# Performance work log

Measured on AMD Instinct MI355X. Metric: run time of the kernel, lower is better.

The kernel has to match this reference:

```python
import jax, jax.numpy as jnp
import numpy as np

N = 100000   # nodes
M = N - 1    # tree edges (child -> parent)
EMB = 512    # embedding_size
ENC = 512    # encoder_size


def setup_inputs() -> dict:
    key = jax.random.key(0)
    ks = jax.random.split(key, 10)
    x = jax.random.normal(ks[0], (N, EMB), jnp.float32)
    h = jax.random.normal(ks[1], (N, ENC), jnp.float32)
    c = jax.random.normal(ks[2], (N, ENC), jnp.float32)
    child_idx = jax.random.randint(ks[3], (M,), 0, N)
    parent_idx = jax.random.randint(ks[4], (M,), 0, N)
    s = 0.05
    W_iou = jax.random.normal(ks[5], (3 * ENC, EMB), jnp.float32) * s
    U_iou = jax.random.normal(ks[6], (3 * ENC, ENC), jnp.float32) * s
    b_iou = jnp.zeros((3 * ENC,), jnp.float32)
    U_f_w = jax.random.normal(ks[7], (ENC, ENC), jnp.float32) * s
    U_f_b = jax.random.normal(ks[8], (ENC,), jnp.float32) * s
    return {"x": x, "h": h, "c": c, "child_idx": child_idx,
            "parent_idx": parent_idx, "W_iou": W_iou, "U_iou": U_iou,
            "b_iou": b_iou, "U_f_w": U_f_w, "U_f_b": U_f_b}


def reference(x, h, c, child_idx, parent_idx, W_iou, U_iou, b_iou, U_f_w, U_f_b):
    n = x.shape[0]
    # message_func: gather child states along edges  [M, ENC]
    h_src = h[child_idx]
    c_src = c[child_idx]
    # reduce_func: forget gate per child, ragged sums over children
    f = jax.nn.sigmoid(h_src @ U_f_w.T + U_f_b)               # [M, ENC]
    h_tilde = jax.ops.segment_sum(h_src, parent_idx, num_segments=n)
    c_red = jax.ops.segment_sum(f * c_src, parent_idx, num_segments=n)
    deg = jax.ops.segment_sum(jnp.ones((h_src.shape[0],), x.dtype),
                              parent_idx, num_segments=n)
    has_child = (deg > 0)[:, None]
    # reduce_func overwrites iou with U_iou(h_tilde) for nodes with children;
    # leaves keep the initial W_iou(x).
    iou = jnp.where(has_child, h_tilde @ U_iou.T, x @ W_iou.T) + b_iou
    i, o, u = jnp.split(iou, 3, axis=1)
    c_new = jax.nn.sigmoid(i) * jnp.tanh(u) + jnp.where(has_child, c_red, 0.0)
    h_new = jax.nn.sigmoid(o) * jnp.tanh(c_new)
    return h_new, c_new
```

## Files before the change

kernel.cpp:

```cpp
#include <hip/hip_runtime.h>
#include <stdint.h>

typedef __bf16 bf16x8 __attribute__((ext_vector_type(8)));
typedef float f32x4 __attribute__((ext_vector_type(4)));
typedef unsigned short ushort8 __attribute__((ext_vector_type(8)));

__device__ __forceinline__ float bf2f(unsigned short u) {
  union { uint32_t i; float f; } v; v.i = ((uint32_t)u) << 16; return v.f;
}
__device__ __forceinline__ unsigned short f2bf(float f) {
  union { uint32_t i; float f; } v; v.f = f;
  uint32_t u = v.i;
  return (unsigned short)((u + 0x7fffu + ((u >> 16) & 1u)) >> 16);
}
__device__ __forceinline__ float sigm(float x) { return 1.0f / (1.0f + __expf(-x)); }
__device__ __forceinline__ float tanh_f(float x) { return 1.0f - 2.0f / (__expf(2.0f * x) + 1.0f); }

__device__ __forceinline__ ushort4 cvt4(float4 a) {
  ushort4 o; o.x = f2bf(a.x); o.y = f2bf(a.y); o.z = f2bf(a.z); o.w = f2bf(a.w); return o;
}

__device__ __forceinline__ int xcd_swz(int bid, int nwg) {
  int q = nwg >> 3, r = nwg & 7;
  int x = bid & 7, idx = bid >> 3;
  return (x < r ? x * (q + 1) : r * (q + 1) + (x - r) * q) + idx;
}

__global__ void k_f2bf(const float* __restrict__ src, unsigned short* __restrict__ dst, long long n8) {
  long long t = (long long)blockIdx.x * blockDim.x + threadIdx.x;
  if (t >= n8) return;
  const float4* s = (const float4*)src + t * 2;
  float4 a = s[0], b = s[1];
  ((ushort4*)dst)[t * 2]     = cvt4(a);
  ((ushort4*)dst)[t * 2 + 1] = cvt4(b);
}

__global__ void k_hist(const int* __restrict__ parent, int* __restrict__ deg, int M) {
  int e = blockIdx.x * blockDim.x + threadIdx.x;
  if (e < M) atomicAdd(&deg[parent[e]], 1);
}

__global__ void k_scan1(const int* __restrict__ deg, unsigned long long* __restrict__ ps,
                        unsigned long long* __restrict__ bsum, int Nn) {
  __shared__ unsigned long long tmp[256];
  int t = blockIdx.x * 256 + threadIdx.x;
  int d = (t < Nn) ? deg[t] : 0;
  unsigned long long v = (unsigned long long)(unsigned)d | ((d > 0) ? (1ull << 32) : 0ull);
  tmp[threadIdx.x] = v;
  __syncthreads();
#pragma unroll
  for (int s = 1; s < 256; s <<= 1) {
    unsigned long long a = (threadIdx.x >= (unsigned)s) ? tmp[threadIdx.x - s] : 0;
    __syncthreads();
    tmp[threadIdx.x] += a;
    __syncthreads();
  }
  if (t < Nn) ps[t] = tmp[threadIdx.x] - v;
  if (threadIdx.x == 255) bsum[blockIdx.x] = tmp[255];
}

__global__ void k_scan2(unsigned long long* __restrict__ bsum, int nb,
                        int* __restrict__ meta, int Nn) {
  __shared__ unsigned long long tmp[512];
  int i = threadIdx.x;
  unsigned long long v = (i < nb) ? bsum[i] : 0;
  tmp[i] = v;
  __syncthreads();
#pragma unroll
  for (int s = 1; s < 512; s <<= 1) {
    unsigned long long a = (i >= s) ? tmp[i - s] : 0;
    __syncthreads();
    tmp[i] += a;
    __syncthreads();
  }
  if (i < nb) bsum[i] = tmp[i] - v;
  if (i == 511) {
    int Ni = (int)(tmp[511] >> 32);
    int L0 = ((Ni + 127) >> 7) << 7;
    meta[0] = Ni;
    meta[1] = L0;
    meta[2] = L0 + (Nn - Ni);
  }
}

__global__ void k_scan3(const unsigned long long* __restrict__ ps,
                        const unsigned long long* __restrict__ bsum,
                        const int* __restrict__ meta, const int* __restrict__ deg,
                        int* __restrict__ rs, int* __restrict__ cursor,
                        int* __restrict__ slot, int Nn) {
  int t = blockIdx.x * 256 + threadIdx.x;
  if (t >= Nn) return;
  unsigned long long p = ps[t] + bsum[blockIdx.x];
  int r  = (int)(p & 0xffffffffull);
  int si = (int)(p >> 32);
  rs[t] = r;
  cursor[t] = r;
  slot[t] = (deg[t] > 0) ? si : (meta[1] + (t - si));
}

__global__ void k_fill(const int* __restrict__ parent, const int* __restrict__ child,
                       int* __restrict__ cursor, int* __restrict__ childlist, int M) {
  int e = blockIdx.x * blockDim.x + threadIdx.x;
  if (e >= M) return;
  int p = parent[e];
  int pos = atomicAdd(&cursor[p], 1);
  childlist[pos] = child[e];
}

__global__ void k_reduce(const unsigned short* __restrict__ hbuf, const float* __restrict__ c,
                         const unsigned short* __restrict__ g, const float* __restrict__ x,
                         const int* __restrict__ rs, const int* __restrict__ childlist,
                         const int* __restrict__ slot,
                         unsigned short* __restrict__ Zp, unsigned short* __restrict__ credb,
                         int Nn, int M) {
  int p = blockIdx.x * 4 + (threadIdx.x >> 6);
  if (p >= Nn) return;
  int ln = threadIdx.x & 63;
  int j = ln * 8;
  int start = rs[p];
  int end = (p + 1 < Nn) ? rs[p + 1] : M;
  size_t zb = (size_t)slot[p] * 512 + j;
  if (end > start) {
    float hs[8] = {0, 0, 0, 0, 0, 0, 0, 0};
    float cs[8] = {0, 0, 0, 0, 0, 0, 0, 0};
    for (int i = start; i < end; ++i) {
      int ch = childlist[i];
      size_t cb = (size_t)ch * 512 + j;
      ushort8 hv = *(const ushort8*)(hbuf + cb);
      ushort8 gv = *(const ushort8*)(g + cb);
      float4 cv0 = *(const float4*)(c + cb);
      float4 cv1 = *(const float4*)(c + cb + 4);
      float cvf[8] = {cv0.x, cv0.y, cv0.z, cv0.w, cv1.x, cv1.y, cv1.z, cv1.w};
#pragma unroll
      for (int q = 0; q < 8; ++q) {
        hs[q] += bf2f(hv[q]);
        cs[q] += bf2f(gv[q]) * cvf[q];
      }
    }
    float4 h0 = {hs[0], hs[1], hs[2], hs[3]}, h1 = {hs[4], hs[5], hs[6], hs[7]};
    float4 c0 = {cs[0], cs[1], cs[2], cs[3]}, c1 = {cs[4], cs[5], cs[6], cs[7]};
    ((ushort4*)(Zp + zb))[0] = cvt4(h0);
    ((ushort4*)(Zp + zb))[1] = cvt4(h1);
    size_t cr = (size_t)p * 512 + j;
    ((ushort4*)(credb + cr))[0] = cvt4(c0);
    ((ushort4*)(credb + cr))[1] = cvt4(c1);
  } else {
    const float4* s = (const float4*)(x + (size_t)p * 512 + j);
    float4 x0 = s[0], x1 = s[1];
    ((ushort4*)(Zp + zb))[0] = cvt4(x0);
    ((ushort4*)(Zp + zb))[1] = cvt4(x1);
  }
}

template <int ACT>
__global__ __launch_bounds__(256)
void k_gemm_bt(const unsigned short* __restrict__ A, int K,
               const unsigned short* __restrict__ Bt,
               const float* __restrict__ bias,
               unsigned short* __restrict__ C, int ldc, int Mrows, int nbx) {
  __shared__ __align__(16) unsigned short ldsA[128 * 32];
  __shared__ __align__(16) unsigned short ldsB[128 * 32];
  const int tid = threadIdx.x;
  const int wv = tid >> 6, ln = tid & 63;
  const int wr = wv >> 1, wc = wv & 1;
  int wg = xcd_swz(blockIdx.x, gridDim.x);
  int rowp = wg / nbx;
  int colp = wg - rowp * nbx;
  const int row0 = rowp * 128;
  const int col0 = colp * 128;

  f32x4 acc[4][4] = {};

  for (int k0 = 0; k0 < K; k0 += 32) {
#pragma unroll
    for (int rep = 0; rep < 2; ++rep) {
      int cidx = rep * 256 + wv * 64 + ln;
      int r  = cidx >> 2;
      int kp = (cidx & 3) * 8;
      int ga = row0 + r; if (ga > Mrows - 1) ga = Mrows - 1;
      const unsigned short* srcA = A + (size_t)ga * K + k0 + kp;
      __builtin_amdgcn_global_load_lds(
          (const __attribute__((address_space(1))) void*)(void*)srcA,
          (__attribute__((address_space(3))) void*)(ldsA + (rep * 256 + wv * 64) * 8),
          16, 0, 0);
      const unsigned short* srcB = Bt + (size_t)(col0 + r) * K + k0 + kp;
      __builtin_amdgcn_global_load_lds(
          (const __attribute__((address_space(1))) void*)(void*)srcB,
          (__attribute__((address_space(3))) void*)(ldsB + (rep * 256 + wv * 64) * 8),
          16, 0, 0);
    }
    __syncthreads();

    bf16x8 af[4], bfr[4];
#pragma unroll
    for (int mi = 0; mi < 4; ++mi)
      af[mi] = *(const bf16x8*)(ldsA + (wr * 64 + mi * 16 + (ln & 15)) * 32 + (ln >> 4) * 8);
#pragma unroll
    for (int ni = 0; ni < 4; ++ni)
      bfr[ni] = *(const bf16x8*)(ldsB + (wc * 64 + ni * 16 + (ln & 15)) * 32 + (ln >> 4) * 8);
#pragma unroll
    for (int mi = 0; mi < 4; ++mi)
#pragma unroll
      for (int ni = 0; ni < 4; ++ni)
        acc[mi][ni] = __builtin_amdgcn_mfma_f32_16x16x32_bf16(af[mi], bfr[ni], acc[mi][ni], 0, 0, 0);
    __syncthreads();
  }

#pragma unroll
  for (int mi = 0; mi < 4; ++mi) {
#pragma unroll
    for (int ni = 0; ni < 4; ++ni) {
      int col = col0 + wc * 64 + ni * 16 + (ln & 15);
      float bv = bias[col];
#pragma unroll
      for (int r = 0; r < 4; ++r) {
        int m = row0 + wr * 64 + mi * 16 + (ln >> 4) * 4 + r;
        if (m < Mrows) {
          float v = acc[mi][ni][r] + bv;
          if (ACT == 1) v = sigm(v);
          C[(size_t)m * ldc + col] = f2bf(v);
        }
      }
    }
  }
}

__global__ __launch_bounds__(256)
void k_gemm_iou(const unsigned short* __restrict__ Zp,
                const unsigned short* __restrict__ Ub,
                const unsigned short* __restrict__ Wb,
                const float* __restrict__ bias,
                const int* __restrict__ meta,
                unsigned short* __restrict__ C) {
  __shared__ __align__(16) unsigned short ldsA[128 * 32];
  __shared__ __align__(16) unsigned short ldsB[128 * 32];
  const int K = 512, ldc = 1536;
  const int tid = threadIdx.x;
  const int wv = tid >> 6, ln = tid & 63;
  const int wr = wv >> 1, wc = wv & 1;
  int wg = xcd_swz(blockIdx.x, gridDim.x);
  int rowp = wg / 12;
  int colp = wg - rowp * 12;
  const int row0 = rowp * 128;
  const int col0 = colp * 128;

  const int Ni = meta[0], L0 = meta[1], lim2 = meta[2];
  const bool internal = row0 < L0;
  const int limit = internal ? Ni : lim2;
  if (row0 >= limit) return;
  const unsigned short* __restrict__ Bt = internal ? Ub : Wb;

  f32x4 acc[4][4] = {};

  for (int k0 = 0; k0 < K; k0 += 32) {
#pragma unroll
    for (int rep = 0; rep < 2; ++rep) {
      int cidx = rep * 256 + wv * 64 + ln;
      int r  = cidx >> 2;
      int kp = (cidx & 3) * 8;
      int ga = row0 + r; if (ga > limit - 1) ga = limit - 1;
      const unsigned short* srcA = Zp + (size_t)ga * K + k0 + kp;
      __builtin_amdgcn_global_load_lds(
          (const __attribute__((address_space(1))) void*)(void*)srcA,
          (__attribute__((address_space(3))) void*)(ldsA + (rep * 256 + wv * 64) * 8),
          16, 0, 0);
      const unsigned short* srcB = Bt + (size_t)(col0 + r) * K + k0 + kp;
      __builtin_amdgcn_global_load_lds(
          (const __attribute__((address_space(1))) void*)(void*)srcB,
          (__attribute__((address_space(3))) void*)(ldsB + (rep * 256 + wv * 64) * 8),
          16, 0, 0);
    }
    __syncthreads();

    bf16x8 af[4], bfr[4];
#pragma unroll
    for (int mi = 0; mi < 4; ++mi)
      af[mi] = *(const bf16x8*)(ldsA + (wr * 64 + mi * 16 + (ln & 15)) * 32 + (ln >> 4) * 8);
#pragma unroll
    for (int ni = 0; ni < 4; ++ni)
      bfr[ni] = *(const bf16x8*)(ldsB + (wc * 64 + ni * 16 + (ln & 15)) * 32 + (ln >> 4) * 8);
#pragma unroll
    for (int mi = 0; mi < 4; ++mi)
#pragma unroll
      for (int ni = 0; ni < 4; ++ni)
        acc[mi][ni] = __builtin_amdgcn_mfma_f32_16x16x32_bf16(af[mi], bfr[ni], acc[mi][ni], 0, 0, 0);
    __syncthreads();
  }

#pragma unroll
  for (int mi = 0; mi < 4; ++mi) {
#pragma unroll
    for (int ni = 0; ni < 4; ++ni) {
      int col = col0 + wc * 64 + ni * 16 + (ln & 15);
      float bv = bias[col];
#pragma unroll
      for (int r = 0; r < 4; ++r) {
        int m = row0 + wr * 64 + mi * 16 + (ln >> 4) * 4 + r;
        if (m < limit) {
          C[(size_t)m * ldc + col] = f2bf(acc[mi][ni][r] + bv);
        }
      }
    }
  }
}

__global__ void k_epilogue(const unsigned short* __restrict__ iou,
                           const unsigned short* __restrict__ credb,
                           const int* __restrict__ slot,
                           const int* __restrict__ meta,
                           float* __restrict__ out, int Nn) {
  long long t = (long long)blockIdx.x * blockDim.x + threadIdx.x;
  int n = (int)(t >> 6);
  if (n >= Nn) return;
  int j = ((int)t & 63) * 8;
  int sl = slot[n];
  int Ni = meta[0];
  size_t ib = (size_t)sl * 1536;
  ushort4 iv0 = *(const ushort4*)(iou + ib + j);
  ushort4 iv1 = *(const ushort4*)(iou + ib + j + 4);
  ushort4 ov0 = *(const ushort4*)(iou + ib + 512 + j);
  ushort4 ov1 = *(const ushort4*)(iou + ib + 512 + j + 4);
  ushort4 uv0 = *(const ushort4*)(iou + ib + 1024 + j);
  ushort4 uv1 = *(const ushort4*)(iou + ib + 1024 + j + 4);

  float carr[8] = {0, 0, 0, 0, 0, 0, 0, 0};
  if (sl < Ni) {
    size_t cr = (size_t)n * 512 + j;
    ushort4 c0 = *(const ushort4*)(credb + cr);
    ushort4 c1 = *(const ushort4*)(credb + cr + 4);
    carr[0] = bf2f(c0.x); carr[1] = bf2f(c0.y); carr[2] = bf2f(c0.z); carr[3] = bf2f(c0.w);
    carr[4] = bf2f(c1.x); carr[5] = bf2f(c1.y); carr[6] = bf2f(c1.z); carr[7] = bf2f(c1.w);
  }

  float iarr[8] = {bf2f(iv0.x), bf2f(iv0.y), bf2f(iv0.z), bf2f(iv0.w),
                   bf2f(iv1.x), bf2f(iv1.y), bf2f(iv1.z), bf2f(iv1.w)};
  float oarr[8] = {bf2f(ov0.x), bf2f(ov0.y), bf2f(ov0.z), bf2f(ov0.w),
                   bf2f(ov1.x), bf2f(ov1.y), bf2f(ov1.z), bf2f(ov1.w)};
  float uarr[8] = {bf2f(uv0.x), bf2f(uv0.y), bf2f(uv0.z), bf2f(uv0.w),
                   bf2f(uv1.x), bf2f(uv1.y), bf2f(uv1.z), bf2f(uv1.w)};
  float hn[8], cn[8];
#pragma unroll
  for (int q = 0; q < 8; ++q) {
    float cc = sigm(iarr[q]) * tanh_f(uarr[q]) + carr[q];
    cn[q] = cc;
    hn[q] = sigm(oarr[q]) * tanh_f(cc);
  }
  size_t hb = (size_t)n * 512 + j;
  size_t cb = (size_t)Nn * 512 + hb;
  *(float4*)(out + hb)     = make_float4(hn[0], hn[1], hn[2], hn[3]);
  *(float4*)(out + hb + 4) = make_float4(hn[4], hn[5], hn[6], hn[7]);
  *(float4*)(out + cb)     = make_float4(cn[0], cn[1], cn[2], cn[3]);
  *(float4*)(out + cb + 4) = make_float4(cn[4], cn[5], cn[6], cn[7]);
}

extern "C" void kernel_launch(void* const* d_in, const int* in_sizes, int n_in,
                              void* d_out, int out_size, void* d_ws, size_t ws_size,
                              hipStream_t stream) {
  const float* x     = (const float*)d_in[0];
  const float* h     = (const float*)d_in[1];
  const float* c     = (const float*)d_in[2];
  const int* child   = (const int*)d_in[3];
  const int* parent  = (const int*)d_in[4];
  const float* W_iou = (const float*)d_in[5];
  const float* U_iou = (const float*)d_in[6];
  const float* b_iou = (const float*)d_in[7];
  const float* U_f_w = (const float*)d_in[8];
  const float* U_f_b = (const float*)d_in[9];

  const int Nn = in_sizes[0] / 512;
  const int M  = in_sizes[3];

  float* out = (float*)d_out;

  char* ws = (char*)d_ws;
  auto al = [](size_t v) { return (v + 255) & ~(size_t)255; };
  size_t sz0    = al((size_t)(Nn + 256) * 1536 * 2);
  size_t offZp  = sz0;
  size_t szZp   = al((size_t)(Nn + 256) * 512 * 2);
  size_t offHb  = offZp + szZp;
  size_t szHb   = al((size_t)Nn * 512 * 2);
  size_t offCr  = offHb + szHb;
  size_t szCr   = al((size_t)Nn * 512 * 2);
  size_t offDeg = offCr + szCr;
  size_t szN4   = al((size_t)Nn * 4);
  size_t offRs  = offDeg + szN4;
  size_t offCur = offRs + szN4;
  size_t offSl  = offCur + szN4;
  size_t offPs  = offSl + szN4;
  size_t szPs   = al((size_t)Nn * 8);
  size_t offCl  = offPs + szPs;
  size_t szCl   = al((size_t)M * 4);
  size_t offBs  = offCl + szCl;
  size_t szBs   = al(512 * 8);
  size_t offMt  = offBs + szBs;
  size_t szMt   = 256;
  size_t offWf  = offMt + szMt;
  size_t szWf   = al(512 * 512 * 2);
  size_t offUb  = offWf + szWf;
  size_t szUw   = al((size_t)1536 * 512 * 2);
  size_t offWb  = offUb + szUw;
  size_t needed = offWb + szUw;
  if (ws_size < needed) return;

  unsigned short* g     = (unsigned short*)(ws);
  unsigned short* iou   = (unsigned short*)(ws);
  unsigned short* Zp    = (unsigned short*)(ws + offZp);
  unsigned short* hbuf  = (unsigned short*)(ws + offHb);
  unsigned short* credb = (unsigned short*)(ws + offCr);
  int*            deg   = (int*)(ws + offDeg);
  int*            rs    = (int*)(ws + offRs);
  int*            cursor= (int*)(ws + offCur);
  int*            slot  = (int*)(ws + offSl);
  unsigned long long* ps   = (unsigned long long*)(ws + offPs);
  int*            clist = (int*)(ws + offCl);
  unsigned long long* bsum = (unsigned long long*)(ws + offBs);
  int*            meta  = (int*)(ws + offMt);
  unsigned short* Wf    = (unsigned short*)(ws + offWf);
  unsigned short* Ub    = (unsigned short*)(ws + offUb);
  unsigned short* Wb    = (unsigned short*)(ws + offWb);

  hipMemsetAsync(deg, 0, (size_t)Nn * 4, stream);

  long long n8h = (long long)Nn * 512 / 8;
  k_f2bf<<<(int)((n8h + 255) / 256), 256, 0, stream>>>(h, hbuf, n8h);
  k_f2bf<<<(512 * 512 / 8 + 255) / 256, 256, 0, stream>>>(U_f_w, Wf, 512 * 512 / 8);
  k_f2bf<<<(1536 * 512 / 8 + 255) / 256, 256, 0, stream>>>(U_iou, Ub, 1536 * 512 / 8);
  k_f2bf<<<(1536 * 512 / 8 + 255) / 256, 256, 0, stream>>>(W_iou, Wb, 1536 * 512 / 8);

  int nb1 = (Nn + 255) / 256;
  k_hist<<<(M + 255) / 256, 256, 0, stream>>>(parent, deg, M);
  k_scan1<<<nb1, 256, 0, stream>>>(deg, ps, bsum, Nn);
  k_scan2<<<1, 512, 0, stream>>>(bsum, nb1, meta, Nn);
  k_scan3<<<nb1, 256, 0, stream>>>(ps, bsum, meta, deg, rs, cursor, slot, Nn);
  k_fill<<<(M + 255) / 256, 256, 0, stream>>>(parent, child, cursor, clist, M);

  int nbyF = (Nn + 127) / 128;
  k_gemm_bt<1><<<nbyF * 4, 256, 0, stream>>>(hbuf, 512, Wf, U_f_b, g, 512, Nn, 4);

  k_reduce<<<(Nn + 3) / 4, 256, 0, stream>>>(hbuf, c, g, x, rs, clist, slot, Zp, credb, Nn, M);

  int nbyI = (Nn >> 7) + 2;
  k_gemm_iou<<<nbyI * 12, 256, 0, stream>>>(Zp, Ub, Wb, b_iou, meta, iou);

  k_epilogue<<<(int)(((long long)Nn * 64 + 255) / 256), 256, 0, stream>>>(iou, credb, slot, meta, out, Nn);
}
```

Measured before the change: 775.6 us.

## Fuse gate epilogue into iou GEMM and pre-multiply forget gate by c

```diff
diff --git a/kernel.cpp b/kernel.cpp
--- a/kernel.cpp
+++ b/kernel.cpp
@@ -33,6 +33,19 @@
   float4 a = s[0], b = s[1];
   ((ushort4*)dst)[t * 2]     = cvt4(a);
   ((ushort4*)dst)[t * 2 + 1] = cvt4(b);
+}
+
+__global__ void k_build_bp(const float* __restrict__ src, unsigned short* __restrict__ bp, int total8) {
+  int t = blockIdx.x * blockDim.x + threadIdx.x;
+  if (t >= total8) return;
+  int R = t >> 6;
+  int ch = t & 63;
+  int g = R / 192, w = R - g * 192;
+  int srow = (w >> 6) * 512 + g * 64 + (w & 63);
+  const float4* s = (const float4*)(src + (size_t)srow * 512 + ch * 8);
+  unsigned short* d = bp + (size_t)R * 512 + ch * 8;
+  ((ushort4*)d)[0] = cvt4(s[0]);
+  ((ushort4*)d)[1] = cvt4(s[1]);
 }
 
 __global__ void k_hist(const int* __restrict__ parent, int* __restrict__ deg, int M) {
@@ -87,7 +100,7 @@
                         const unsigned long long* __restrict__ bsum,
                         const int* __restrict__ meta, const int* __restrict__ deg,
                         int* __restrict__ rs, int* __restrict__ cursor,
-                        int* __restrict__ slot, int Nn) {
+                        int* __restrict__ slot, int* __restrict__ nodeof, int Nn) {
   int t = blockIdx.x * 256 + threadIdx.x;
   if (t >= Nn) return;
   unsigned long long p = ps[t] + bsum[blockIdx.x];
@@ -95,7 +108,9 @@
   int si = (int)(p >> 32);
   rs[t] = r;
   cursor[t] = r;
-  slot[t] = (deg[t] > 0) ? si : (meta[1] + (t - si));
+  int sl = (deg[t] > 0) ? si : (meta[1] + (t - si));
+  slot[t] = sl;
+  nodeof[sl] = t;
 }
 
 __global__ void k_fill(const int* __restrict__ parent, const int* __restrict__ child,
@@ -107,8 +122,8 @@
   childlist[pos] = child[e];
 }
 
-__global__ void k_reduce(const unsigned short* __restrict__ hbuf, const float* __restrict__ c,
-                         const unsigned short* __restrict__ g, const float* __restrict__ x,
+__global__ void k_reduce(const unsigned short* __restrict__ hbuf,
+                         const unsigned short* __restrict__ fcb, const float* __restrict__ x,
                          const int* __restrict__ rs, const int* __restrict__ childlist,
                          const int* __restrict__ slot,
                          unsigned short* __restrict__ Zp, unsigned short* __restrict__ credb,
@@ -127,23 +142,19 @@
       int ch = childlist[i];
       size_t cb = (size_t)ch * 512 + j;
       ushort8 hv = *(const ushort8*)(hbuf + cb);
-      ushort8 gv = *(const ushort8*)(g + cb);
-      float4 cv0 = *(const float4*)(c + cb);
-      float4 cv1 = *(const float4*)(c + cb + 4);
-      float cvf[8] = {cv0.x, cv0.y, cv0.z, cv0.w, cv1.x, cv1.y, cv1.z, cv1.w};
+      ushort8 fv = *(const ushort8*)(fcb + cb);
 #pragma unroll
       for (int q = 0; q < 8; ++q) {
         hs[q] += bf2f(hv[q]);
-        cs[q] += bf2f(gv[q]) * cvf[q];
+        cs[q] += bf2f(fv[q]);
       }
     }
     float4 h0 = {hs[0], hs[1], hs[2], hs[3]}, h1 = {hs[4], hs[5], hs[6], hs[7]};
     float4 c0 = {cs[0], cs[1], cs[2], cs[3]}, c1 = {cs[4], cs[5], cs[6], cs[7]};
     ((ushort4*)(Zp + zb))[0] = cvt4(h0);
     ((ushort4*)(Zp + zb))[1] = cvt4(h1);
-    size_t cr = (size_t)p * 512 + j;
-    ((ushort4*)(credb + cr))[0] = cvt4(c0);
-    ((ushort4*)(credb + cr))[1] = cvt4(c1);
+    ((ushort4*)(credb + zb))[0] = cvt4(c0);
+    ((ushort4*)(credb + zb))[1] = cvt4(c1);
   } else {
     const float4* s = (const float4*)(x + (size_t)p * 512 + j);
     float4 x0 = s[0], x1 = s[1];
@@ -152,20 +163,20 @@
   }
 }
 
-template <int ACT>
 __global__ __launch_bounds__(256)
-void k_gemm_bt(const unsigned short* __restrict__ A, int K,
-               const unsigned short* __restrict__ Bt,
-               const float* __restrict__ bias,
-               unsigned short* __restrict__ C, int ldc, int Mrows, int nbx) {
+void k_gemm_f(const unsigned short* __restrict__ A,
+              const unsigned short* __restrict__ Bt,
+              const float* __restrict__ bias, const float* __restrict__ cmat,
+              unsigned short* __restrict__ C, int Mrows) {
   __shared__ __align__(16) unsigned short ldsA[128 * 32];
   __shared__ __align__(16) unsigned short ldsB[128 * 32];
+  const int K = 512, ldc = 512;
   const int tid = threadIdx.x;
   const int wv = tid >> 6, ln = tid & 63;
   const int wr = wv >> 1, wc = wv & 1;
   int wg = xcd_swz(blockIdx.x, gridDim.x);
-  int rowp = wg / nbx;
-  int colp = wg - rowp * nbx;
+  int rowp = wg >> 2;
+  int colp = wg & 3;
   const int row0 = rowp * 128;
   const int col0 = colp * 128;
 
@@ -216,8 +227,7 @@
       for (int r = 0; r < 4; ++r) {
         int m = row0 + wr * 64 + mi * 16 + (ln >> 4) * 4 + r;
         if (m < Mrows) {
-          float v = acc[mi][ni][r] + bv;
-          if (ACT == 1) v = sigm(v);
+          float v = sigm(acc[mi][ni][r] + bv) * cmat[(size_t)m * ldc + col];
           C[(size_t)m * ldc + col] = f2bf(v);
         }
       }
@@ -226,131 +236,105 @@
 }
 
 __global__ __launch_bounds__(256)
-void k_gemm_iou(const unsigned short* __restrict__ Zp,
-                const unsigned short* __restrict__ Ub,
-                const unsigned short* __restrict__ Wb,
-                const float* __restrict__ bias,
-                const int* __restrict__ meta,
-                unsigned short* __restrict__ C) {
+void k_gemm_iou_fused(const unsigned short* __restrict__ Zp,
+                      const unsigned short* __restrict__ BpU,
+                      const unsigned short* __restrict__ BpW,
+                      const float* __restrict__ bias,
+                      const int* __restrict__ meta,
+                      const int* __restrict__ nodeof,
+                      const unsigned short* __restrict__ credb,
+                      float* __restrict__ out, int Nn) {
   __shared__ __align__(16) unsigned short ldsA[128 * 32];
-  __shared__ __align__(16) unsigned short ldsB[128 * 32];
-  const int K = 512, ldc = 1536;
+  __shared__ __align__(16) unsigned short ldsB[192 * 32];
+  const int K = 512;
   const int tid = threadIdx.x;
   const int wv = tid >> 6, ln = tid & 63;
-  const int wr = wv >> 1, wc = wv & 1;
   int wg = xcd_swz(blockIdx.x, gridDim.x);
-  int rowp = wg / 12;
-  int colp = wg - rowp * 12;
+  int rowp = wg >> 3;
+  int colp = wg & 7;
   const int row0 = rowp * 128;
-  const int col0 = colp * 128;
+  const int enc0 = colp * 64;
 
   const int Ni = meta[0], L0 = meta[1], lim2 = meta[2];
   const bool internal = row0 < L0;
   const int limit = internal ? Ni : lim2;
   if (row0 >= limit) return;
-  const unsigned short* __restrict__ Bt = internal ? Ub : Wb;
-
-  f32x4 acc[4][4] = {};
+  const unsigned short* __restrict__ Bp = internal ? BpU : BpW;
+
+  f32x4 acc[2][12] = {};
 
   for (int k0 = 0; k0 < K; k0 += 32) {
 #pragma unroll
     for (int rep = 0; rep < 2; ++rep) {
-      int cidx = rep * 256 + wv * 64 + ln;
+      int cidx = rep * 256 + tid;
       int r  = cidx >> 2;
       int kp = (cidx & 3) * 8;
       int ga = row0 + r; if (ga > limit - 1) ga = limit - 1;
       const unsigned short* srcA = Zp + (size_t)ga * K + k0 + kp;
       __builtin_amdgcn_global_load_lds(
           (const __attribute__((address_space(1))) void*)(void*)srcA,
-          (__attribute__((address_space(3))) void*)(ldsA + (rep * 256 + wv * 64) * 8),
+          (__attribute__((address_space(3))) void*)(ldsA + (size_t)cidx * 8),
           16, 0, 0);
-      const unsigned short* srcB = Bt + (size_t)(col0 + r) * K + k0 + kp;
+    }
+#pragma unroll
+    for (int rep = 0; rep < 3; ++rep) {
+      int cidx = rep * 256 + tid;
+      int r  = cidx >> 2;
+      int kp = (cidx & 3) * 8;
+      const unsigned short* srcB = Bp + (size_t)(colp * 192 + r) * K + k0 + kp;
       __builtin_amdgcn_global_load_lds(
           (const __attribute__((address_space(1))) void*)(void*)srcB,
-          (__attribute__((address_space(3))) void*)(ldsB + (rep * 256 + wv * 64) * 8),
+          (__attribute__((address_space(3))) void*)(ldsB + (size_t)cidx * 8),
           16, 0, 0);
     }
     __syncthreads();
 
-    bf16x8 af[4], bfr[4];
-#pragma unroll
-    for (int mi = 0; mi < 4; ++mi)
-      af[mi] = *(const bf16x8*)(ldsA + (wr * 64 + mi * 16 + (ln & 15)) * 32 + (ln >> 4) * 8);
-#pragma unroll
-    for (int ni = 0; ni < 4; ++ni)
-      bfr[ni] = *(const bf16x8*)(ldsB + (wc * 64 + ni * 16 + (ln & 15)) * 32 + (ln >> 4) * 8);
-#pragma unroll
-    for (int mi = 0; mi < 4; ++mi)
-#pragma unroll
-      for (int ni = 0; ni < 4; ++ni)
+    bf16x8 af[2], bfr[12];
+#pragma unroll
+    for (int mi = 0; mi < 2; ++mi)
+      af[mi] = *(const bf16x8*)(ldsA + (wv * 32 + mi * 16 + (ln & 15)) * 32 + (ln >> 4) * 8);
+#pragma unroll
+    for (int ni = 0; ni < 12; ++ni)
+      bfr[ni] = *(const bf16x8*)(ldsB + (ni * 16 + (ln & 15)) * 32 + (ln >> 4) * 8);
+#pragma unroll
+    for (int mi = 0; mi < 2; ++mi)
+#pragma unroll
+      for (int ni = 0; ni < 12; ++ni)
         acc[mi][ni] = __builtin_amdgcn_mfma_f32_16x16x32_bf16(af[mi], bfr[ni], acc[mi][ni], 0, 0, 0);
     __syncthreads();
   }
 
-#pragma unroll
-  for (int mi = 0; mi < 4; ++mi) {
-#pragma unroll
-    for (int ni = 0; ni < 4; ++ni) {
-      int col = col0 + wc * 64 + ni * 16 + (ln & 15);
-      float bv = bias[col];
-#pragma unroll
-      for (int r = 0; r < 4; ++r) {
-        int m = row0 + wr * 64 + mi * 16 + (ln >> 4) * 4 + r;
-        if (m < limit) {
-          C[(size_t)m * ldc + col] = f2bf(acc[mi][ni][r] + bv);
-        }
+  float bi[4], bo[4], bu[4];
+#pragma unroll
+  for (int f = 0; f < 4; ++f) {
+    int enc = enc0 + f * 16 + (ln & 15);
+    bi[f] = bias[enc];
+    bo[f] = bias[512 + enc];
+    bu[f] = bias[1024 + enc];
+  }
+  const size_t cOff = (size_t)Nn * 512;
+#pragma unroll
+  for (int mi = 0; mi < 2; ++mi) {
+#pragma unroll
+    for (int r = 0; r < 4; ++r) {
+      int m = row0 + wv * 32 + mi * 16 + (ln >> 4) * 4 + r;
+      if (m >= limit) continue;
+      int node = nodeof[m];
+      size_t ob = (size_t)node * 512 + enc0 + (ln & 15);
+#pragma unroll
+      for (int f = 0; f < 4; ++f) {
+        float iv = acc[mi][f][r] + bi[f];
+        float ov = acc[mi][4 + f][r] + bo[f];
+        float uv = acc[mi][8 + f][r] + bu[f];
+        float cred = 0.0f;
+        if (internal) cred = bf2f(credb[(size_t)m * 512 + enc0 + f * 16 + (ln & 15)]);
+        float cc = sigm(iv) * tanh_f(uv) + cred;
+        float hn = sigm(ov) * tanh_f(cc);
+        out[ob + f * 16] = hn;
+        out[cOff + ob + f * 16] = cc;
       }
     }
   }
-}
-
-__global__ void k_epilogue(const unsigned short* __restrict__ iou,
-                           const unsigned short* __restrict__ credb,
-                           const int* __restrict__ slot,
-                           const int* __restrict__ meta,
-                           float* __restrict__ out, int Nn) {
-  long long t = (long long)blockIdx.x * blockDim.x + threadIdx.x;
-  int n = (int)(t >> 6);
-  if (n >= Nn) return;
-  int j = ((int)t & 63) * 8;
-  int sl = slot[n];
-  int Ni = meta[0];
-  size_t ib = (size_t)sl * 1536;
-  ushort4 iv0 = *(const ushort4*)(iou + ib + j);
-  ushort4 iv1 = *(const ushort4*)(iou + ib + j + 4);
-  ushort4 ov0 = *(const ushort4*)(iou + ib + 512 + j);
-  ushort4 ov1 = *(const ushort4*)(iou + ib + 512 + j + 4);
-  ushort4 uv0 = *(const ushort4*)(iou + ib + 1024 + j);
-  ushort4 uv1 = *(const ushort4*)(iou + ib + 1024 + j + 4);
-
-  float carr[8] = {0, 0, 0, 0, 0, 0, 0, 0};
-  if (sl < Ni) {
-    size_t cr = (size_t)n * 512 + j;
-    ushort4 c0 = *(const ushort4*)(credb + cr);
-    ushort4 c1 = *(const ushort4*)(credb + cr + 4);
-    carr[0] = bf2f(c0.x); carr[1] = bf2f(c0.y); carr[2] = bf2f(c0.z); carr[3] = bf2f(c0.w);
-    carr[4] = bf2f(c1.x); carr[5] = bf2f(c1.y); carr[6] = bf2f(c1.z); carr[7] = bf2f(c1.w);
-  }
-
-  float iarr[8] = {bf2f(iv0.x), bf2f(iv0.y), bf2f(iv0.z), bf2f(iv0.w),
-                   bf2f(iv1.x), bf2f(iv1.y), bf2f(iv1.z), bf2f(iv1.w)};
-  float oarr[8] = {bf2f(ov0.x), bf2f(ov0.y), bf2f(ov0.z), bf2f(ov0.w),
-                   bf2f(ov1.x), bf2f(ov1.y), bf2f(ov1.z), bf2f(ov1.w)};
-  float uarr[8] = {bf2f(uv0.x), bf2f(uv0.y), bf2f(uv0.z), bf2f(uv0.w),
-                   bf2f(uv1.x), bf2f(uv1.y), bf2f(uv1.z), bf2f(uv1.w)};
-  float hn[8], cn[8];
-#pragma unroll
-  for (int q = 0; q < 8; ++q) {
-    float cc = sigm(iarr[q]) * tanh_f(uarr[q]) + carr[q];
-    cn[q] = cc;
-    hn[q] = sigm(oarr[q]) * tanh_f(cc);
-  }
-  size_t hb = (size_t)n * 512 + j;
-  size_t cb = (size_t)Nn * 512 + hb;
-  *(float4*)(out + hb)     = make_float4(hn[0], hn[1], hn[2], hn[3]);
-  *(float4*)(out + hb + 4) = make_float4(hn[4], hn[5], hn[6], hn[7]);
-  *(float4*)(out + cb)     = make_float4(cn[0], cn[1], cn[2], cn[3]);
-  *(float4*)(out + cb + 4) = make_float4(cn[4], cn[5], cn[6], cn[7]);
 }
 
 extern "C" void kernel_launch(void* const* d_in, const int* in_sizes, int n_in,
@@ -374,19 +358,21 @@
 
   char* ws = (char*)d_ws;
   auto al = [](size_t v) { return (v + 255) & ~(size_t)255; };
-  size_t sz0    = al((size_t)(Nn + 256) * 1536 * 2);
-  size_t offZp  = sz0;
+  size_t szFc   = al((size_t)Nn * 512 * 2);
+  size_t offZp  = szFc;
   size_t szZp   = al((size_t)(Nn + 256) * 512 * 2);
   size_t offHb  = offZp + szZp;
   size_t szHb   = al((size_t)Nn * 512 * 2);
   size_t offCr  = offHb + szHb;
-  size_t szCr   = al((size_t)Nn * 512 * 2);
+  size_t szCr   = al((size_t)(Nn + 256) * 512 * 2);
   size_t offDeg = offCr + szCr;
   size_t szN4   = al((size_t)Nn * 4);
   size_t offRs  = offDeg + szN4;
   size_t offCur = offRs + szN4;
   size_t offSl  = offCur + szN4;
-  size_t offPs  = offSl + szN4;
+  size_t offNo  = offSl + szN4;
+  size_t szNo   = al((size_t)(Nn + 256) * 4);
+  size_t offPs  = offNo + szNo;
   size_t szPs   = al((size_t)Nn * 8);
   size_t offCl  = offPs + szPs;
   size_t szCl   = al((size_t)M * 4);
@@ -402,8 +388,7 @@
   size_t needed = offWb + szUw;
   if (ws_size < needed) return;
 
-  unsigned short* g     = (unsigned short*)(ws);
-  unsigned short* iou   = (unsigned short*)(ws);
+  unsigned short* fcb   = (unsigned short*)(ws);
   unsigned short* Zp    = (unsigned short*)(ws + offZp);
   unsigned short* hbuf  = (unsigned short*)(ws + offHb);
   unsigned short* credb = (unsigned short*)(ws + offCr);
@@ -411,36 +396,35 @@
   int*            rs    = (int*)(ws + offRs);
   int*            cursor= (int*)(ws + offCur);
   int*            slot  = (int*)(ws + offSl);
+  int*            nodeof= (int*)(ws + offNo);
   unsigned long long* ps   = (unsigned long long*)(ws + offPs);
   int*            clist = (int*)(ws + offCl);
   unsigned long long* bsum = (unsigned long long*)(ws + offBs);
   int*            meta  = (int*)(ws + offMt);
   unsigned short* Wf    = (unsigned short*)(ws + offWf);
-  unsigned short* Ub    = (unsigned short*)(ws + offUb);
-  unsigned short* Wb    = (unsigned short*)(ws + offWb);
+  unsigned short* BpU   = (unsigned short*)(ws + offUb);
+  unsigned short* BpW   = (unsigned short*)(ws + offWb);
 
   hipMemsetAsync(deg, 0, (size_t)Nn * 4, stream);
 
   long long n8h = (long long)Nn * 512 / 8;
   k_f2bf<<<(int)((n8h + 255) / 256), 256, 0, stream>>>(h, hbuf, n8h);
   k_f2bf<<<(512 * 512 / 8 + 255) / 256, 256, 0, stream>>>(U_f_w, Wf, 512 * 512 / 8);
-  k_f2bf<<<(1536 * 512 / 8 + 255) / 256, 256, 0, stream>>>(U_iou, Ub, 1536 * 512 / 8);
-  k_f2bf<<<(1536 * 512 / 8 + 255) / 256, 256, 0, stream>>>(W_iou, Wb, 1536 * 512 / 8);
+  k_build_bp<<<(1536 * 64 + 255) / 256, 256, 0, stream>>>(U_iou, BpU, 1536 * 64);
+  k_build_bp<<<(1536 * 64 + 255) / 256, 256, 0, stream>>>(W_iou, BpW, 1536 * 64);
 
   int nb1 = (Nn + 255) / 256;
   k_hist<<<(M + 255) / 256, 256, 0, stream>>>(parent, deg, M);
   k_scan1<<<nb1, 256, 0, stream>>>(deg, ps, bsum, Nn);
   k_scan2<<<1, 512, 0, stream>>>(bsum, nb1, meta, Nn);
-  k_scan3<<<nb1, 256, 0, stream>>>(ps, bsum, meta, deg, rs, cursor, slot, Nn);
+  k_scan3<<<nb1, 256, 0, stream>>>(ps, bsum, meta, deg, rs, cursor, slot, nodeof, Nn);
   k_fill<<<(M + 255) / 256, 256, 0, stream>>>(parent, child, cursor, clist, M);
 
   int nbyF = (Nn + 127) / 128;
-  k_gemm_bt<1><<<nbyF * 4, 256, 0, stream>>>(hbuf, 512, Wf, U_f_b, g, 512, Nn, 4);
-
-  k_reduce<<<(Nn + 3) / 4, 256, 0, stream>>>(hbuf, c, g, x, rs, clist, slot, Zp, credb, Nn, M);
+  k_gemm_f<<<nbyF * 4, 256, 0, stream>>>(hbuf, Wf, U_f_b, c, fcb, Nn);
+
+  k_reduce<<<(Nn + 3) / 4, 256, 0, stream>>>(hbuf, fcb, x, rs, clist, slot, Zp, credb, Nn, M);
 
   int nbyI = (Nn >> 7) + 2;
-  k_gemm_iou<<<nbyI * 12, 256, 0, stream>>>(Zp, Ub, Wb, b_iou, meta, iou);
-
-  k_epilogue<<<(int)(((long long)Nn * 64 + 255) / 256), 256, 0, stream>>>(iou, credb, slot, meta, out, Nn);
-}
+  k_gemm_iou_fused<<<nbyI * 8, 256, 0, stream>>>(Zp, BpU, BpW, b_iou, meta, nodeof, credb, out, Nn);
+}
```

New measurement: 852.3 us. 1.1x slower.

## Fuse forget-gate product into GEMM epilogue and scatter iou rows by node

Applied to the files above, without the earlier changes.

```diff
diff --git a/kernel.cpp b/kernel.cpp
--- a/kernel.cpp
+++ b/kernel.cpp
@@ -87,7 +87,7 @@
                         const unsigned long long* __restrict__ bsum,
                         const int* __restrict__ meta, const int* __restrict__ deg,
                         int* __restrict__ rs, int* __restrict__ cursor,
-                        int* __restrict__ slot, int Nn) {
+                        int* __restrict__ slot, int* __restrict__ nodeof, int Nn) {
   int t = blockIdx.x * 256 + threadIdx.x;
   if (t >= Nn) return;
   unsigned long long p = ps[t] + bsum[blockIdx.x];
@@ -95,7 +95,9 @@
   int si = (int)(p >> 32);
   rs[t] = r;
   cursor[t] = r;
-  slot[t] = (deg[t] > 0) ? si : (meta[1] + (t - si));
+  int sl = (deg[t] > 0) ? si : (meta[1] + (t - si));
+  slot[t] = sl;
+  nodeof[sl] = t;
 }
 
 __global__ void k_fill(const int* __restrict__ parent, const int* __restrict__ child,
@@ -107,8 +109,8 @@
   childlist[pos] = child[e];
 }
 
-__global__ void k_reduce(const unsigned short* __restrict__ hbuf, const float* __restrict__ c,
-                         const unsigned short* __restrict__ g, const float* __restrict__ x,
+__global__ void k_reduce(const unsigned short* __restrict__ hbuf,
+                         const unsigned short* __restrict__ fcb, const float* __restrict__ x,
                          const int* __restrict__ rs, const int* __restrict__ childlist,
                          const int* __restrict__ slot,
                          unsigned short* __restrict__ Zp, unsigned short* __restrict__ credb,
@@ -127,14 +129,11 @@
       int ch = childlist[i];
       size_t cb = (size_t)ch * 512 + j;
       ushort8 hv = *(const ushort8*)(hbuf + cb);
-      ushort8 gv = *(const ushort8*)(g + cb);
-      float4 cv0 = *(const float4*)(c + cb);
-      float4 cv1 = *(const float4*)(c + cb + 4);
-      float cvf[8] = {cv0.x, cv0.y, cv0.z, cv0.w, cv1.x, cv1.y, cv1.z, cv1.w};
+      ushort8 fv = *(const ushort8*)(fcb + cb);
 #pragma unroll
       for (int q = 0; q < 8; ++q) {
         hs[q] += bf2f(hv[q]);
-        cs[q] += bf2f(gv[q]) * cvf[q];
+        cs[q] += bf2f(fv[q]);
       }
     }
     float4 h0 = {hs[0], hs[1], hs[2], hs[3]}, h1 = {hs[4], hs[5], hs[6], hs[7]};
@@ -152,20 +151,20 @@
   }
 }
 
-template <int ACT>
 __global__ __launch_bounds__(256)
-void k_gemm_bt(const unsigned short* __restrict__ A, int K,
-               const unsigned short* __restrict__ Bt,
-               const float* __restrict__ bias,
-               unsigned short* __restrict__ C, int ldc, int Mrows, int nbx) {
+void k_gemm_f(const unsigned short* __restrict__ A,
+              const unsigned short* __restrict__ Bt,
+              const float* __restrict__ bias, const float* __restrict__ cmat,
+              unsigned short* __restrict__ C, int Mrows) {
   __shared__ __align__(16) unsigned short ldsA[128 * 32];
   __shared__ __align__(16) unsigned short ldsB[128 * 32];
+  const int K = 512, ldc = 512;
   const int tid = threadIdx.x;
   const int wv = tid >> 6, ln = tid & 63;
   const int wr = wv >> 1, wc = wv & 1;
   int wg = xcd_swz(blockIdx.x, gridDim.x);
-  int rowp = wg / nbx;
-  int colp = wg - rowp * nbx;
+  int rowp = wg >> 2;
+  int colp = wg & 3;
   const int row0 = rowp * 128;
   const int col0 = colp * 128;
 
@@ -202,25 +201,25 @@
     for (int mi = 0; mi < 4; ++mi)
 #pragma unroll
       for (int ni = 0; ni < 4; ++ni)
-        acc[mi][ni] = __builtin_amdgcn_mfma_f32_16x16x32_bf16(af[mi], bfr[ni], acc[mi][ni], 0, 0, 0);
+        acc[mi][ni] = __builtin_amdgcn_mfma_f32_16x16x32_bf16(bfr[ni], af[mi], acc[mi][ni], 0, 0, 0);
     __syncthreads();
   }
 
 #pragma unroll
   for (int mi = 0; mi < 4; ++mi) {
+    int gm = row0 + wr * 64 + mi * 16 + (ln & 15);
+    if (gm >= Mrows) continue;
 #pragma unroll
     for (int ni = 0; ni < 4; ++ni) {
-      int col = col0 + wc * 64 + ni * 16 + (ln & 15);
-      float bv = bias[col];
-#pragma unroll
-      for (int r = 0; r < 4; ++r) {
-        int m = row0 + wr * 64 + mi * 16 + (ln >> 4) * 4 + r;
-        if (m < Mrows) {
-          float v = acc[mi][ni][r] + bv;
-          if (ACT == 1) v = sigm(v);
-          C[(size_t)m * ldc + col] = f2bf(v);
-        }
-      }
+      int gn = col0 + wc * 64 + ni * 16 + (ln >> 4) * 4;
+      float4 bv = *(const float4*)(bias + gn);
+      float4 cv = *(const float4*)(cmat + (size_t)gm * ldc + gn);
+      ushort4 o;
+      o.x = f2bf(sigm(acc[mi][ni][0] + bv.x) * cv.x);
+      o.y = f2bf(sigm(acc[mi][ni][1] + bv.y) * cv.y);
+      o.z = f2bf(sigm(acc[mi][ni][2] + bv.z) * cv.z);
+      o.w = f2bf(sigm(acc[mi][ni][3] + bv.w) * cv.w);
+      *(ushort4*)(C + (size_t)gm * ldc + gn) = o;
     }
   }
 }
@@ -231,6 +230,7 @@
                 const unsigned short* __restrict__ Wb,
                 const float* __restrict__ bias,
                 const int* __restrict__ meta,
+                const int* __restrict__ nodeof,
                 unsigned short* __restrict__ C) {
   __shared__ __align__(16) unsigned short ldsA[128 * 32];
   __shared__ __align__(16) unsigned short ldsB[128 * 32];
@@ -283,39 +283,39 @@
     for (int mi = 0; mi < 4; ++mi)
 #pragma unroll
       for (int ni = 0; ni < 4; ++ni)
-        acc[mi][ni] = __builtin_amdgcn_mfma_f32_16x16x32_bf16(af[mi], bfr[ni], acc[mi][ni], 0, 0, 0);
+        acc[mi][ni] = __builtin_amdgcn_mfma_f32_16x16x32_bf16(bfr[ni], af[mi], acc[mi][ni], 0, 0, 0);
     __syncthreads();
   }
 
 #pragma unroll
   for (int mi = 0; mi < 4; ++mi) {
+    int m = row0 + wr * 64 + mi * 16 + (ln & 15);
+    if (m >= limit) continue;
+    int node = nodeof[m];
+    size_t ob = (size_t)node * ldc;
 #pragma unroll
     for (int ni = 0; ni < 4; ++ni) {
-      int col = col0 + wc * 64 + ni * 16 + (ln & 15);
-      float bv = bias[col];
-#pragma unroll
-      for (int r = 0; r < 4; ++r) {
-        int m = row0 + wr * 64 + mi * 16 + (ln >> 4) * 4 + r;
-        if (m < limit) {
-          C[(size_t)m * ldc + col] = f2bf(acc[mi][ni][r] + bv);
-        }
-      }
+      int gn = col0 + wc * 64 + ni * 16 + (ln >> 4) * 4;
+      float4 bv = *(const float4*)(bias + gn);
+      ushort4 o;
+      o.x = f2bf(acc[mi][ni][0] + bv.x);
+      o.y = f2bf(acc[mi][ni][1] + bv.y);
+      o.z = f2bf(acc[mi][ni][2] + bv.z);
+      o.w = f2bf(acc[mi][ni][3] + bv.w);
+      *(ushort4*)(C + ob + gn) = o;
     }
   }
 }
 
 __global__ void k_epilogue(const unsigned short* __restrict__ iou,
                            const unsigned short* __restrict__ credb,
-                           const int* __restrict__ slot,
-                           const int* __restrict__ meta,
+                           const int* __restrict__ deg,
                            float* __restrict__ out, int Nn) {
   long long t = (long long)blockIdx.x * blockDim.x + threadIdx.x;
   int n = (int)(t >> 6);
   if (n >= Nn) return;
   int j = ((int)t & 63) * 8;
-  int sl = slot[n];
-  int Ni = meta[0];
-  size_t ib = (size_t)sl * 1536;
+  size_t ib = (size_t)n * 1536;
   ushort4 iv0 = *(const ushort4*)(iou + ib + j);
   ushort4 iv1 = *(const ushort4*)(iou + ib + j + 4);
   ushort4 ov0 = *(const ushort4*)(iou + ib + 512 + j);
@@ -324,7 +324,7 @@
   ushort4 uv1 = *(const ushort4*)(iou + ib + 1024 + j + 4);
 
   float carr[8] = {0, 0, 0, 0, 0, 0, 0, 0};
-  if (sl < Ni) {
+  if (deg[n] > 0) {
     size_t cr = (size_t)n * 512 + j;
     ushort4 c0 = *(const ushort4*)(credb + cr);
     ushort4 c1 = *(const ushort4*)(credb + cr + 4);
@@ -374,7 +374,7 @@
 
   char* ws = (char*)d_ws;
   auto al = [](size_t v) { return (v + 255) & ~(size_t)255; };
-  size_t sz0    = al((size_t)(Nn + 256) * 1536 * 2);
+  size_t sz0    = al((size_t)Nn * 1536 * 2);
   size_t offZp  = sz0;
   size_t szZp   = al((size_t)(Nn + 256) * 512 * 2);
   size_t offHb  = offZp + szZp;
@@ -386,7 +386,9 @@
   size_t offRs  = offDeg + szN4;
   size_t offCur = offRs + szN4;
   size_t offSl  = offCur + szN4;
-  size_t offPs  = offSl + szN4;
+  size_t offNo  = offSl + szN4;
+  size_t szNo   = al((size_t)(Nn + 256) * 4);
+  size_t offPs  = offNo + szNo;
   size_t szPs   = al((size_t)Nn * 8);
   size_t offCl  = offPs + szPs;
   size_t szCl   = al((size_t)M * 4);
@@ -402,7 +404,7 @@
   size_t needed = offWb + szUw;
   if (ws_size < needed) return;
 
-  unsigned short* g     = (unsigned short*)(ws);
+  unsigned short* fcb   = (unsigned short*)(ws);
   unsigned short* iou   = (unsigned short*)(ws);
   unsigned short* Zp    = (unsigned short*)(ws + offZp);
   unsigned short* hbuf  = (unsigned short*)(ws + offHb);
@@ -411,6 +413,7 @@
   int*            rs    = (int*)(ws + offRs);
   int*            cursor= (int*)(ws + offCur);
   int*            slot  = (int*)(ws + offSl);
+  int*            nodeof= (int*)(ws + offNo);
   unsigned long long* ps   = (unsigned long long*)(ws + offPs);
   int*            clist = (int*)(ws + offCl);
   unsigned long long* bsum = (unsigned long long*)(ws + offBs);
@@ -431,16 +434,16 @@
   k_hist<<<(M + 255) / 256, 256, 0, stream>>>(parent, deg, M);
   k_scan1<<<nb1, 256, 0, stream>>>(deg, ps, bsum, Nn);
   k_scan2<<<1, 512, 0, stream>>>(bsum, nb1, meta, Nn);
-  k_scan3<<<nb1, 256, 0, stream>>>(ps, bsum, meta, deg, rs, cursor, slot, Nn);
+  k_scan3<<<nb1, 256, 0, stream>>>(ps, bsum, meta, deg, rs, cursor, slot, nodeof, Nn);
   k_fill<<<(M + 255) / 256, 256, 0, stream>>>(parent, child, cursor, clist, M);
 
   int nbyF = (Nn + 127) / 128;
-  k_gemm_bt<1><<<nbyF * 4, 256, 0, stream>>>(hbuf, 512, Wf, U_f_b, g, 512, Nn, 4);
-
-  k_reduce<<<(Nn + 3) / 4, 256, 0, stream>>>(hbuf, c, g, x, rs, clist, slot, Zp, credb, Nn, M);
+  k_gemm_f<<<nbyF * 4, 256, 0, stream>>>(hbuf, Wf, U_f_b, c, fcb, Nn);
+
+  k_reduce<<<(Nn + 3) / 4, 256, 0, stream>>>(hbuf, fcb, x, rs, clist, slot, Zp, credb, Nn, M);
 
   int nbyI = (Nn >> 7) + 2;
-  k_gemm_iou<<<nbyI * 12, 256, 0, stream>>>(Zp, Ub, Wb, b_iou, meta, iou);
-
-  k_epilogue<<<(int)(((long long)Nn * 64 + 255) / 256), 256, 0, stream>>>(iou, credb, slot, meta, out, Nn);
-}
+  k_gemm_iou<<<nbyI * 12, 256, 0, stream>>>(Zp, Ub, Wb, b_iou, meta, nodeof, iou);
+
+  k_epilogue<<<(int)(((long long)Nn * 64 + 255) / 256), 256, 0, stream>>>(iou, credb, deg, out, Nn);
+}
```

Result: faster. 736.0 us (-5.1%).
